# Optimization experiments

Hardware: AMD Instinct MI355X
Metric: run time of the kernel (lower is better)

Reference implementation:

```python
import jax, jax.numpy as jnp
import numpy as np

TEX = 256  # texture grid resolution hardcoded in the module


def _grid_sample_bilinear(img, grid):
    """torch.F.grid_sample(img, grid): bilinear, zero padding, align_corners=False.
    img: [B,C,H,W]; grid: [B,Hg,Wg,2] in [-1,1] (x,y order). Returns [B,C,Hg,Wg]."""
    B, C, H, W = img.shape
    gx = (grid[..., 0] + 1.0) * (W * 0.5) - 0.5  # pixel-space x
    gy = (grid[..., 1] + 1.0) * (H * 0.5) - 0.5  # pixel-space y
    x0 = jnp.floor(gx)
    y0 = jnp.floor(gy)
    wx1 = gx - x0
    wy1 = gy - y0

    def corner(xi, yi, w):
        valid = (xi >= 0) & (xi <= W - 1) & (yi >= 0) & (yi <= H - 1)
        xc = jnp.clip(xi, 0, W - 1).astype(jnp.int32)
        yc = jnp.clip(yi, 0, H - 1).astype(jnp.int32)
        # per-batch gather: [B,C,Hg,Wg]
        v = jax.vmap(lambda im, yy, xx: im[:, yy, xx])(img, yc, xc)
        return v * (w * valid.astype(img.dtype))[:, None, :, :]

    return (corner(x0, y0, (1 - wx1) * (1 - wy1))
            + corner(x0 + 1, y0, wx1 * (1 - wy1))
            + corner(x0, y0 + 1, (1 - wx1) * wy1)
            + corner(x0 + 1, y0 + 1, wx1 * wy1))


def setup_inputs() -> dict:
    key = jax.random.key(0)
    k1, k2, k3, k4, k5, k6 = jax.random.split(key, 6)
    B, V, P, HW = 16, 5023, 60000, 512
    source_img = jax.random.uniform(k1, (B, 3, HW, HW), dtype=jnp.float32)
    target_mesh_v = jax.random.normal(k2, (B, V, 3), dtype=jnp.float32) * 0.1
    vertex_normals = jax.random.normal(k3, (B, V, 3), dtype=jnp.float32)
    # camera: [scale, tx, ty]; scale near 8-10 typical for DECA crops, keep ~1 range here
    camera_params = jnp.concatenate([
        jax.random.uniform(k4, (B, 1), minval=5.0, maxval=10.0),
        jax.random.uniform(k4, (B, 2), minval=-0.05, maxval=0.05)], axis=1).astype(jnp.float32)
    valid_pixel_3d_faces = jax.random.randint(k5, (P, 3), 0, V, dtype=jnp.int32)
    bc = jax.random.uniform(k6, (P, 3), dtype=jnp.float32) + 1e-3
    valid_pixel_b_coords = bc / jnp.sum(bc, axis=1, keepdims=True)  # barycentric
    lin = jnp.arange(P, dtype=jnp.int32)  # collision-free texel enumeration
    x_coords = lin % TEX
    y_coords = lin // TEX
    return {"source_img": source_img, "target_mesh_v": target_mesh_v,
            "vertex_normals": vertex_normals, "camera_params": camera_params,
            "valid_pixel_3d_faces": valid_pixel_3d_faces,
            "valid_pixel_b_coords": valid_pixel_b_coords,
            "x_coords": x_coords, "y_coords": y_coords}


def reference(source_img, target_mesh_v, vertex_normals, camera_params,
              valid_pixel_3d_faces, valid_pixel_b_coords, x_coords, y_coords):
    B = source_img.shape[0]
    # gather face vertices and barycentric-interpolate: [B,P,3(verts),3(xyz)] -> [B,P,3]
    tv = target_mesh_v[:, valid_pixel_3d_faces, :]
    pixel_3d_points = jnp.einsum('bpkc,pk->bpc', tv, valid_pixel_b_coords)
    # batch_orth_proj: scale * (xy + txy); then flip y
    cam = camera_params[:, None, :]  # [B,1,3]
    proj_xy = cam[..., 0:1] * (pixel_3d_points[..., :2] + cam[..., 1:3])
    proj_xy = jnp.stack([proj_xy[..., 0], -proj_xy[..., 1]], axis=-1)  # [B,P,2]
    # scatter into 256x256 sampling grid (zeros elsewhere)
    texture_grid = jnp.zeros((B, TEX, TEX, 2), dtype=jnp.float32)
    texture_grid = texture_grid.at[:, y_coords, x_coords, :].set(proj_xy)
    texture_img = _grid_sample_bilinear(source_img, texture_grid)  # [B,3,256,256]
    # interpolated normal z-component for visibility
    nvz = vertex_normals[..., 2][:, valid_pixel_3d_faces]  # [B,P,3]
    pixel_nz = jnp.einsum('bpk,pk->bp', nvz, valid_pixel_b_coords)
    texture_vis_mask = jnp.zeros((B, 1, TEX, TEX), dtype=jnp.bool_)
    texture_vis_mask = texture_vis_mask.at[:, 0, y_coords, x_coords].set(pixel_nz < 0)
    return texture_img, texture_vis_mask
```

## Files before the change

### kernel.cpp

```cpp
#include <hip/hip_runtime.h>
#include <math.h>

#define TEXD 256
#define NT (TEXD * TEXD)
#define BB 16
#define NPAIR (BB / 2)

struct alignas(4) F3 { float x, y, z; };
struct alignas(4) I3 { int a, b, c; };

__global__ void flame_prep_kernel(const int* __restrict__ xs,
                                  const int* __restrict__ ys,
                                  int* __restrict__ map, int P,
                                  const float* __restrict__ tmv,
                                  const float* __restrict__ vn,
                                  float4* __restrict__ pv, int V,
                                  const float* __restrict__ img,
                                  uchar4* __restrict__ img8,
                                  int HW, int mapBlocks, int packBlocks) {
    int bid = blockIdx.x;
    if (bid < mapBlocks) {
        int p = bid * 256 + threadIdx.x;
        if (p < P) map[ys[p] * TEXD + xs[p]] = p;
    } else if (bid < mapBlocks + packBlocks) {
        int i = (bid - mapBlocks) * 256 + threadIdx.x;
        if (i < BB * V) {
            int b = i / V;
            int v = i - b * V;
            pv[(size_t)v * BB + b] =
                make_float4(tmv[(size_t)i * 3 + 0], tmv[(size_t)i * 3 + 1],
                            vn[(size_t)i * 3 + 2], 0.0f);
        }
    } else {
        int plane = HW * HW;
        int cb = bid - mapBlocks - packBlocks;
        int pb = plane / 256;
        int b = cb / pb;
        int off = (cb - b * pb) * 256 + threadIdx.x;
        const float* base = img + (size_t)b * 3 * plane;
        float r = base[off];
        float g = base[off + plane];
        float bl = base[off + 2 * plane];
        img8[(size_t)b * plane + off] =
            make_uchar4((unsigned char)__float2int_rn(r * 255.0f),
                        (unsigned char)__float2int_rn(g * 255.0f),
                        (unsigned char)__float2int_rn(bl * 255.0f), 0);
    }
}

__global__ void flame_project_kernel(const float4* __restrict__ pv,
                                     const float* __restrict__ cam,
                                     const I3* __restrict__ faces,
                                     const F3* __restrict__ bcw,
                                     const int* __restrict__ map,
                                     float4* __restrict__ gridpair,
                                     float* __restrict__ out_mask) {
    int gid = blockIdx.x * 256 + threadIdx.x;
    int t = gid >> 2;
    int q = gid & 3;
    int p = map[t];

    int bs0 = 2 * q;
    int bs1 = 2 * q + 1;

    float gx[4], gy[4], mk[4];
    if (p >= 0) {
        I3 f3 = faces[p];
        F3 w3 = bcw[p];
        const float4* ra = pv + (size_t)f3.a * BB;
        const float4* rb = pv + (size_t)f3.b * BB;
        const float4* rc = pv + (size_t)f3.c * BB;
#pragma unroll
        for (int j = 0; j < 4; ++j) {
            int b = (j & 1) ? (2 * q + 1) : (2 * q);
            if (j >= 2) b += NPAIR;
            float4 A = ra[b];
            float4 Bv = rb[b];
            float4 C = rc[b];
            float px = A.x * w3.x + Bv.x * w3.y + C.x * w3.z;
            float py = A.y * w3.x + Bv.y * w3.y + C.y * w3.z;
            float nz = A.z * w3.x + Bv.z * w3.y + C.z * w3.z;
            float fo = cam[b * 3 + 0];
            float cx = cam[b * 3 + 1];
            float cy = cam[b * 3 + 2];
            gx[j] = fo * (px + cx);
            gy[j] = -(fo * (py + cy));
            mk[j] = (nz < 0.0f) ? 1.0f : 0.0f;
        }
    } else {
#pragma unroll
        for (int j = 0; j < 4; ++j) { gx[j] = 0.0f; gy[j] = 0.0f; mk[j] = 0.0f; }
    }

    gridpair[(size_t)bs0 * NT + t] = make_float4(gx[0], gy[0], gx[2], gy[2]);
    gridpair[(size_t)bs1 * NT + t] = make_float4(gx[1], gy[1], gx[3], gy[3]);
    out_mask[(size_t)bs0 * NT + t] = mk[0];
    out_mask[(size_t)bs1 * NT + t] = mk[1];
    out_mask[(size_t)(bs0 + NPAIR) * NT + t] = mk[2];
    out_mask[(size_t)(bs1 + NPAIR) * NT + t] = mk[3];
}

__device__ __forceinline__ void sample3_u8(const uchar4* __restrict__ base,
                                           int HW, float gxn, float gyn,
                                           float out[3]) {
    float half = 0.5f * (float)HW;
    float gx = (gxn + 1.0f) * half - 0.5f;
    float gy = (gyn + 1.0f) * half - 0.5f;

    float x0f = floorf(gx);
    float y0f = floorf(gy);
    float wx = gx - x0f;
    float wy = gy - y0f;
    int x0 = (int)x0f;
    int y0 = (int)y0f;
    int x1 = x0 + 1;
    int y1 = y0 + 1;

    bool vx0 = (x0 >= 0) && (x0 <= HW - 1);
    bool vx1 = (x1 >= 0) && (x1 <= HW - 1);
    bool vy0 = (y0 >= 0) && (y0 <= HW - 1);
    bool vy1 = (y1 >= 0) && (y1 <= HW - 1);

    const float s = 1.0f / 255.0f;
    float w00 = (1.0f - wx) * (1.0f - wy) * ((vx0 && vy0) ? s : 0.0f);
    float w01 = wx * (1.0f - wy) * ((vx1 && vy0) ? s : 0.0f);
    float w10 = (1.0f - wx) * wy * ((vx0 && vy1) ? s : 0.0f);
    float w11 = wx * wy * ((vx1 && vy1) ? s : 0.0f);

    int xb = min(max(x0, 0), HW - 2);
    bool lo = (x0 == xb);
    float wl0 = lo ? w00 : w01;
    float wh0 = lo ? w01 : w00;
    float wl1 = lo ? w10 : w11;
    float wh1 = lo ? w11 : w10;

    int cy0 = min(max(y0, 0), HW - 1);
    int cy1 = min(max(y1, 0), HW - 1);
    const uchar4* r0 = base + (size_t)cy0 * HW + xb;
    const uchar4* r1 = base + (size_t)cy1 * HW + xb;
    uchar4 a0 = r0[0], a1 = r0[1];
    uchar4 d0 = r1[0], d1 = r1[1];

    out[0] = a0.x * wl0 + a1.x * wh0 + d0.x * wl1 + d1.x * wh1;
    out[1] = a0.y * wl0 + a1.y * wh0 + d0.y * wl1 + d1.y * wh1;
    out[2] = a0.z * wl0 + a1.z * wh0 + d0.z * wl1 + d1.z * wh1;
}

__global__ void flame_gather_kernel(const uchar4* __restrict__ img8,
                                    const float4* __restrict__ gridpair,
                                    float* __restrict__ out_img,
                                    int HW) {
    int pair = blockIdx.x % NPAIR;
    int tile = blockIdx.x / NPAIR;
    int t = tile * 256 + threadIdx.x;

    float4 g = gridpair[(size_t)pair * NT + t];
    int b0 = pair;
    int b1 = pair + NPAIR;
    size_t plane = (size_t)HW * HW;

    float o0[3], o1[3];
    sample3_u8(img8 + (size_t)b0 * plane, HW, g.x, g.y, o0);
    sample3_u8(img8 + (size_t)b1 * plane, HW, g.z, g.w, o1);

#pragma unroll
    for (int c = 0; c < 3; ++c) {
        __builtin_nontemporal_store(o0[c], out_img + ((size_t)(b0 * 3 + c)) * NT + t);
        __builtin_nontemporal_store(o1[c], out_img + ((size_t)(b1 * 3 + c)) * NT + t);
    }
}

extern "C" void kernel_launch(void* const* d_in, const int* in_sizes, int n_in,
                              void* d_out, int out_size, void* d_ws, size_t ws_size,
                              hipStream_t stream) {
    const float* source_img = (const float*)d_in[0];
    const float* tmv        = (const float*)d_in[1];
    const float* vn         = (const float*)d_in[2];
    const float* cam        = (const float*)d_in[3];
    const int*   faces      = (const int*)d_in[4];
    const float* bcw        = (const float*)d_in[5];
    const int*   xs         = (const int*)d_in[6];
    const int*   ys         = (const int*)d_in[7];

    int B = in_sizes[3] / 3;
    int P = in_sizes[4] / 3;
    int V = in_sizes[1] / (3 * B);
    int HW = (int)(sqrt((double)(in_sizes[0] / (3 * B))) + 0.5);

    char* wsb = (char*)d_ws;
    int* map = (int*)wsb;
    wsb += (size_t)NT * sizeof(int);
    float4* pv = (float4*)wsb;
    wsb += (size_t)B * V * sizeof(float4);
    float4* gridpair = (float4*)wsb;
    wsb += (size_t)NPAIR * NT * sizeof(float4);
    uchar4* img8 = (uchar4*)wsb;

    float* out_img = (float*)d_out;
    float* out_mask = out_img + (size_t)B * 3 * NT;

    hipMemsetAsync(map, 0xFF, (size_t)NT * sizeof(int), stream);

    int mapBlocks = (P + 255) / 256;
    int packBlocks = (B * V + 255) / 256;
    int convBlocks = B * (HW * HW / 256);
    flame_prep_kernel<<<mapBlocks + packBlocks + convBlocks, 256, 0, stream>>>(
        xs, ys, map, P, tmv, vn, pv, V, source_img, img8, HW, mapBlocks, packBlocks);

    flame_project_kernel<<<4 * NT / 256, 256, 0, stream>>>(
        pv, cam, (const I3*)faces, (const F3*)bcw, map, gridpair, out_mask);

    flame_gather_kernel<<<NPAIR * (NT / 256), 256, 0, stream>>>(
        img8, gridpair, out_img, HW);
}
```

Before: 121.7 us.

## Move image u8 conversion into projection kernel, split small prep kernel

Splits the prep kernel so the small map/vertex-pack work runs first on its own, and the large float-to-u8 image conversion now shares a launch with the projection blocks. The conversion no longer sits in front of the projection on the critical path and the two can overlap. Mask stores become nontemporal, and the bilinear sampler fetches each pair of adjacent texels with one 8-byte load instead of two 4-byte loads. The 8-byte load is only 4-byte aligned, and the launch count is unchanged.

Result: slower. 125.0 us (+2.7%).

```diff
diff --git a/kernel.cpp b/kernel.cpp
--- a/kernel.cpp
+++ b/kernel.cpp
@@ -8,21 +8,20 @@
 
 struct alignas(4) F3 { float x, y, z; };
 struct alignas(4) I3 { int a, b, c; };
-
-__global__ void flame_prep_kernel(const int* __restrict__ xs,
-                                  const int* __restrict__ ys,
-                                  int* __restrict__ map, int P,
-                                  const float* __restrict__ tmv,
-                                  const float* __restrict__ vn,
-                                  float4* __restrict__ pv, int V,
-                                  const float* __restrict__ img,
-                                  uchar4* __restrict__ img8,
-                                  int HW, int mapBlocks, int packBlocks) {
+struct alignas(4) U8P { uchar4 a, b; };
+
+__global__ void flame_prep_small_kernel(const int* __restrict__ xs,
+                                        const int* __restrict__ ys,
+                                        int* __restrict__ map, int P,
+                                        const float* __restrict__ tmv,
+                                        const float* __restrict__ vn,
+                                        float4* __restrict__ pv, int V,
+                                        int mapBlocks) {
     int bid = blockIdx.x;
     if (bid < mapBlocks) {
         int p = bid * 256 + threadIdx.x;
         if (p < P) map[ys[p] * TEXD + xs[p]] = p;
-    } else if (bid < mapBlocks + packBlocks) {
+    } else {
         int i = (bid - mapBlocks) * 256 + threadIdx.x;
         if (i < BB * V) {
             int b = i / V;
@@ -31,9 +30,67 @@
                 make_float4(tmv[(size_t)i * 3 + 0], tmv[(size_t)i * 3 + 1],
                             vn[(size_t)i * 3 + 2], 0.0f);
         }
+    }
+}
+
+__global__ void flame_mega_kernel(const float4* __restrict__ pv,
+                                  const float* __restrict__ cam,
+                                  const I3* __restrict__ faces,
+                                  const F3* __restrict__ bcw,
+                                  const int* __restrict__ map,
+                                  float4* __restrict__ gridpair,
+                                  float* __restrict__ out_mask,
+                                  const float* __restrict__ img,
+                                  uchar4* __restrict__ img8,
+                                  int HW, int projBlocks) {
+    int bid = blockIdx.x;
+    if (bid < projBlocks) {
+        int gid = bid * 256 + threadIdx.x;
+        int t = gid >> 2;
+        int q = gid & 3;
+        int p = map[t];
+
+        int bs0 = 2 * q;
+        int bs1 = 2 * q + 1;
+
+        float gx[4], gy[4], mk[4];
+        if (p >= 0) {
+            I3 f3 = faces[p];
+            F3 w3 = bcw[p];
+            const float4* ra = pv + (size_t)f3.a * BB;
+            const float4* rb = pv + (size_t)f3.b * BB;
+            const float4* rc = pv + (size_t)f3.c * BB;
+#pragma unroll
+            for (int j = 0; j < 4; ++j) {
+                int b = (j & 1) ? bs1 : bs0;
+                if (j >= 2) b += NPAIR;
+                float4 A = ra[b];
+                float4 Bv = rb[b];
+                float4 C = rc[b];
+                float px = A.x * w3.x + Bv.x * w3.y + C.x * w3.z;
+                float py = A.y * w3.x + Bv.y * w3.y + C.y * w3.z;
+                float nz = A.z * w3.x + Bv.z * w3.y + C.z * w3.z;
+                float fo = cam[b * 3 + 0];
+                float cx = cam[b * 3 + 1];
+                float cy = cam[b * 3 + 2];
+                gx[j] = fo * (px + cx);
+                gy[j] = -(fo * (py + cy));
+                mk[j] = (nz < 0.0f) ? 1.0f : 0.0f;
+            }
+        } else {
+#pragma unroll
+            for (int j = 0; j < 4; ++j) { gx[j] = 0.0f; gy[j] = 0.0f; mk[j] = 0.0f; }
+        }
+
+        gridpair[(size_t)bs0 * NT + t] = make_float4(gx[0], gy[0], gx[2], gy[2]);
+        gridpair[(size_t)bs1 * NT + t] = make_float4(gx[1], gy[1], gx[3], gy[3]);
+        __builtin_nontemporal_store(mk[0], out_mask + (size_t)bs0 * NT + t);
+        __builtin_nontemporal_store(mk[1], out_mask + (size_t)bs1 * NT + t);
+        __builtin_nontemporal_store(mk[2], out_mask + (size_t)(bs0 + NPAIR) * NT + t);
+        __builtin_nontemporal_store(mk[3], out_mask + (size_t)(bs1 + NPAIR) * NT + t);
     } else {
         int plane = HW * HW;
-        int cb = bid - mapBlocks - packBlocks;
+        int cb = bid - projBlocks;
         int pb = plane / 256;
         int b = cb / pb;
         int off = (cb - b * pb) * 256 + threadIdx.x;
@@ -48,58 +105,6 @@
     }
 }
 
-__global__ void flame_project_kernel(const float4* __restrict__ pv,
-                                     const float* __restrict__ cam,
-                                     const I3* __restrict__ faces,
-                                     const F3* __restrict__ bcw,
-                                     const int* __restrict__ map,
-                                     float4* __restrict__ gridpair,
-                                     float* __restrict__ out_mask) {
-    int gid = blockIdx.x * 256 + threadIdx.x;
-    int t = gid >> 2;
-    int q = gid & 3;
-    int p = map[t];
-
-    int bs0 = 2 * q;
-    int bs1 = 2 * q + 1;
-
-    float gx[4], gy[4], mk[4];
-    if (p >= 0) {
-        I3 f3 = faces[p];
-        F3 w3 = bcw[p];
-        const float4* ra = pv + (size_t)f3.a * BB;
-        const float4* rb = pv + (size_t)f3.b * BB;
-        const float4* rc = pv + (size_t)f3.c * BB;
-#pragma unroll
-        for (int j = 0; j < 4; ++j) {
-            int b = (j & 1) ? (2 * q + 1) : (2 * q);
-            if (j >= 2) b += NPAIR;
-            float4 A = ra[b];
-            float4 Bv = rb[b];
-            float4 C = rc[b];
-            float px = A.x * w3.x + Bv.x * w3.y + C.x * w3.z;
-            float py = A.y * w3.x + Bv.y * w3.y + C.y * w3.z;
-            float nz = A.z * w3.x + Bv.z * w3.y + C.z * w3.z;
-            float fo = cam[b * 3 + 0];
-            float cx = cam[b * 3 + 1];
-            float cy = cam[b * 3 + 2];
-            gx[j] = fo * (px + cx);
-            gy[j] = -(fo * (py + cy));
-            mk[j] = (nz < 0.0f) ? 1.0f : 0.0f;
-        }
-    } else {
-#pragma unroll
-        for (int j = 0; j < 4; ++j) { gx[j] = 0.0f; gy[j] = 0.0f; mk[j] = 0.0f; }
-    }
-
-    gridpair[(size_t)bs0 * NT + t] = make_float4(gx[0], gy[0], gx[2], gy[2]);
-    gridpair[(size_t)bs1 * NT + t] = make_float4(gx[1], gy[1], gx[3], gy[3]);
-    out_mask[(size_t)bs0 * NT + t] = mk[0];
-    out_mask[(size_t)bs1 * NT + t] = mk[1];
-    out_mask[(size_t)(bs0 + NPAIR) * NT + t] = mk[2];
-    out_mask[(size_t)(bs1 + NPAIR) * NT + t] = mk[3];
-}
-
 __device__ __forceinline__ void sample3_u8(const uchar4* __restrict__ base,
                                            int HW, float gxn, float gyn,
                                            float out[3]) {
@@ -136,14 +141,12 @@
 
     int cy0 = min(max(y0, 0), HW - 1);
     int cy1 = min(max(y1, 0), HW - 1);
-    const uchar4* r0 = base + (size_t)cy0 * HW + xb;
-    const uchar4* r1 = base + (size_t)cy1 * HW + xb;
-    uchar4 a0 = r0[0], a1 = r0[1];
-    uchar4 d0 = r1[0], d1 = r1[1];
-
-    out[0] = a0.x * wl0 + a1.x * wh0 + d0.x * wl1 + d1.x * wh1;
-    out[1] = a0.y * wl0 + a1.y * wh0 + d0.y * wl1 + d1.y * wh1;
-    out[2] = a0.z * wl0 + a1.z * wh0 + d0.z * wl1 + d1.z * wh1;
+    U8P p0 = *(const U8P*)(base + (size_t)cy0 * HW + xb);
+    U8P p1 = *(const U8P*)(base + (size_t)cy1 * HW + xb);
+
+    out[0] = p0.a.x * wl0 + p0.b.x * wh0 + p1.a.x * wl1 + p1.b.x * wh1;
+    out[1] = p0.a.y * wl0 + p0.b.y * wh0 + p1.a.y * wl1 + p1.b.y * wh1;
+    out[2] = p0.a.z * wl0 + p0.b.z * wh0 + p1.a.z * wl1 + p1.b.z * wh1;
 }
 
 __global__ void flame_gather_kernel(const uchar4* __restrict__ img8,
@@ -203,12 +206,14 @@
 
     int mapBlocks = (P + 255) / 256;
     int packBlocks = (B * V + 255) / 256;
+    flame_prep_small_kernel<<<mapBlocks + packBlocks, 256, 0, stream>>>(
+        xs, ys, map, P, tmv, vn, pv, V, mapBlocks);
+
+    int projBlocks = 4 * NT / 256;
     int convBlocks = B * (HW * HW / 256);
-    flame_prep_kernel<<<mapBlocks + packBlocks + convBlocks, 256, 0, stream>>>(
-        xs, ys, map, P, tmv, vn, pv, V, source_img, img8, HW, mapBlocks, packBlocks);
-
-    flame_project_kernel<<<4 * NT / 256, 256, 0, stream>>>(
-        pv, cam, (const I3*)faces, (const F3*)bcw, map, gridpair, out_mask);
+    flame_mega_kernel<<<projBlocks + convBlocks, 256, 0, stream>>>(
+        pv, cam, (const I3*)faces, (const F3*)bcw, map, gridpair, out_mask,
+        source_img, img8, HW, projBlocks);
 
     flame_gather_kernel<<<NPAIR * (NT / 256), 256, 0, stream>>>(
         img8, gridpair, out_img, HW);
```
